# Kernel optimization log

Hardware: AMD Instinct MI355X
Metric: run time of the kernel (lower is better)

Reference implementation:

```python
import jax, jax.numpy as jnp
import numpy as np

EPS = 1e-10


def _sqdist(emb):
    # emb: [B, F, N]; pairwise squared distance over (eta, phi) rows 1:3
    coord = emb[:, 1:3, :]  # [B, 2, N]
    diff = coord[:, :, :, None] - coord[:, :, None, :]  # [B, 2, N, N]
    return jnp.sum(diff * diff, axis=1)  # [B, N, N]


def setup_inputs() -> dict:
    key = jax.random.key(0)
    k1, k2, k3 = jax.random.split(key, 3)
    B, F, N = 8, 6, 2048
    emb = jax.random.uniform(k1, (B, F, N), dtype=jnp.float32) + 0.1  # positive momenta
    alpha = 1.0 * (jax.random.uniform(k2, (1, 1), dtype=jnp.float32) * 0.02 + 0.99)
    beta = 1.0 * (jax.random.uniform(k3, (1, 1, 1), dtype=jnp.float32) * 0.02 + 0.99)
    return {"emb": emb, "alpha": alpha, "beta": beta}


def reference(emb, alpha, beta):
    # emb: [B, F, N]; alpha: [1,1]; beta: [1,1,1]
    sqdist = _sqdist(emb)                                  # [B, N, N]
    momentum = emb[:, 4, :] + EPS                          # [B, N]
    pow_momenta = jnp.exp(2.0 * alpha * jnp.log(momentum)) # p^(2*alpha), [B, N]
    # symmetric pairwise min: min(p_i^{2a}, p_j^{2a})
    min_momenta = jnp.minimum(pow_momenta[:, :, None], pow_momenta[:, None, :])  # [B, N, N]
    d_ij_alpha = sqdist * min_momenta
    d_ij_norm = -(beta ** 2) * d_ij_alpha                  # broadcast [1,1,1]
    # original unbind/cat/softmax/chunk/stack == row-wise softmax over last dim
    w_ij = jax.nn.softmax(d_ij_norm, axis=-1)
    return w_ij
```

## Files before the change

### kernel.cpp

```cpp
#include <hip/hip_runtime.h>

#define Nn   2048
#define BLK  256
#define TI   16
#define EPSf 1e-10f

typedef float f32x4 __attribute__((ext_vector_type(4)));

__global__ __launch_bounds__(BLK) void qcd_softmax_kernel(
    const float* __restrict__ emb,
    const float* __restrict__ alpha_p,
    const float* __restrict__ beta_p,
    float* __restrict__ out)
{
    __shared__ float s_cx[TI], s_cy[TI], s_q[TI];
    __shared__ float s_red[2][4];

    const int t  = threadIdx.x;
    const int b  = blockIdx.x >> 7;
    const int i0 = (blockIdx.x & 127) * TI;

    const float twoalpha = 2.0f * alpha_p[0];
    const float beta     = beta_p[0];
    const float nb2l2e   = -(beta * beta) * 1.4426950408889634f;

    const float* eb = emb + (size_t)b * 6 * Nn;

    const int j0 = t * 4;
    const int j1 = j0 + 1024;

    f32x4 cjx0 = *(const f32x4*)(eb + 1 * Nn + j0);
    f32x4 cjx1 = *(const f32x4*)(eb + 1 * Nn + j1);
    f32x4 cjy0 = *(const f32x4*)(eb + 2 * Nn + j0);
    f32x4 cjy1 = *(const f32x4*)(eb + 2 * Nn + j1);
    f32x4 mm0  = *(const f32x4*)(eb + 4 * Nn + j0);
    f32x4 mm1  = *(const f32x4*)(eb + 4 * Nn + j1);

    float qj0[4], qj1[4];
#pragma unroll
    for (int k = 0; k < 4; ++k) {
        qj0[k] = nb2l2e * expf(twoalpha * logf(mm0[k] + EPSf));
        qj1[k] = nb2l2e * expf(twoalpha * logf(mm1[k] + EPSf));
    }

    if (t < TI) {
        const int i = i0 + t;
        s_cx[t] = eb[1 * Nn + i];
        s_cy[t] = eb[2 * Nn + i];
        s_q[t]  = nb2l2e * expf(twoalpha * logf(eb[4 * Nn + i] + EPSf));
    }
    __syncthreads();

    const int wid  = t >> 6;
    const int lane = t & 63;

    for (int r = 0; r < TI; ++r) {
        const float cix = s_cx[r];
        const float ciy = s_cy[r];
        const float qi  = s_q[r];

        float e[8];
        float lsum = 0.f;
#pragma unroll
        for (int k = 0; k < 4; ++k) {
            const float dx = cjx0[k] - cix;
            const float dy = cjy0[k] - ciy;
            const float d2 = fmaf(dy, dy, dx * dx);
            e[k] = __builtin_amdgcn_exp2f(d2 * fmaxf(qj0[k], qi));
            lsum += e[k];
        }
#pragma unroll
        for (int k = 0; k < 4; ++k) {
            const float dx = cjx1[k] - cix;
            const float dy = cjy1[k] - ciy;
            const float d2 = fmaf(dy, dy, dx * dx);
            e[4 + k] = __builtin_amdgcn_exp2f(d2 * fmaxf(qj1[k], qi));
            lsum += e[4 + k];
        }

#pragma unroll
        for (int off = 32; off > 0; off >>= 1)
            lsum += __shfl_xor(lsum, off, 64);

        const int buf = r & 1;
        if (lane == 0) s_red[buf][wid] = lsum;
        __syncthreads();
        const float tot  = s_red[buf][0] + s_red[buf][1] + s_red[buf][2] + s_red[buf][3];
        const float rinv = 1.0f / tot;

        float* orow = out + (((size_t)b * Nn) + (size_t)(i0 + r)) * Nn;
        f32x4 o0, o1;
#pragma unroll
        for (int k = 0; k < 4; ++k) {
            o0[k] = e[k] * rinv;
            o1[k] = e[4 + k] * rinv;
        }
        __builtin_nontemporal_store(o0, (f32x4*)(orow + j0));
        __builtin_nontemporal_store(o1, (f32x4*)(orow + j1));
    }
}

extern "C" void kernel_launch(void* const* d_in, const int* in_sizes, int n_in,
                              void* d_out, int out_size, void* d_ws, size_t ws_size,
                              hipStream_t stream) {
    const float* emb   = (const float*)d_in[0];
    const float* alpha = (const float*)d_in[1];
    const float* beta  = (const float*)d_in[2];
    float* out         = (float*)d_out;

    dim3 grid(8 * (Nn / TI));
    dim3 block(BLK);
    qcd_softmax_kernel<<<grid, block, 0, stream>>>(emb, alpha, beta, out);
}
```

Baseline: 149.0 us.

## Assign whole rows per wavefront to drop block-level softmax reduction barriers

Each wavefront now owns four full output rows and holds all 2048 column coordinates and powered momenta in registers, so the row sum is reduced with wave shuffles only. This removes the shared-memory exchange and the __syncthreads per row. Nontemporal stores become plain stores, and launch bounds ask for two blocks per SIMD. The cost is much higher register use (96 floats of column state per thread) and the column exp/log setup repeated by every wave.

```diff
diff --git a/kernel.cpp b/kernel.cpp
--- a/kernel.cpp
+++ b/kernel.cpp
@@ -1,102 +1,87 @@
 #include <hip/hip_runtime.h>
 
 #define Nn   2048
-#define BLK  256
-#define TI   16
+#define NB   8
 #define EPSf 1e-10f
+#define RPW  4
+#define WPB  4
+#define BLK  (WPB * 64)
 
 typedef float f32x4 __attribute__((ext_vector_type(4)));
 
-__global__ __launch_bounds__(BLK) void qcd_softmax_kernel(
+__global__ __launch_bounds__(BLK, 2) void qcd_softmax_kernel(
     const float* __restrict__ emb,
     const float* __restrict__ alpha_p,
     const float* __restrict__ beta_p,
     float* __restrict__ out)
 {
-    __shared__ float s_cx[TI], s_cy[TI], s_q[TI];
-    __shared__ float s_red[2][4];
+    const int t    = threadIdx.x;
+    const int lane = t & 63;
+    const int w    = t >> 6;
+    const int b    = blockIdx.x >> 7;
+    const int i0   = (blockIdx.x & 127) * (RPW * WPB) + w * RPW;
 
-    const int t  = threadIdx.x;
-    const int b  = blockIdx.x >> 7;
-    const int i0 = (blockIdx.x & 127) * TI;
+    const float* eb  = emb + (size_t)b * 6 * Nn;
+    const float* cxp = eb + 1 * Nn;
+    const float* cyp = eb + 2 * Nn;
+    const float* mp  = eb + 4 * Nn;
 
     const float twoalpha = 2.0f * alpha_p[0];
     const float beta     = beta_p[0];
     const float nb2l2e   = -(beta * beta) * 1.4426950408889634f;
 
-    const float* eb = emb + (size_t)b * 6 * Nn;
-
-    const int j0 = t * 4;
-    const int j1 = j0 + 1024;
-
-    f32x4 cjx0 = *(const f32x4*)(eb + 1 * Nn + j0);
-    f32x4 cjx1 = *(const f32x4*)(eb + 1 * Nn + j1);
-    f32x4 cjy0 = *(const f32x4*)(eb + 2 * Nn + j0);
-    f32x4 cjy1 = *(const f32x4*)(eb + 2 * Nn + j1);
-    f32x4 mm0  = *(const f32x4*)(eb + 4 * Nn + j0);
-    f32x4 mm1  = *(const f32x4*)(eb + 4 * Nn + j1);
-
-    float qj0[4], qj1[4];
+    f32x4 cjx[8], cjy[8], qj[8];
 #pragma unroll
-    for (int k = 0; k < 4; ++k) {
-        qj0[k] = nb2l2e * expf(twoalpha * logf(mm0[k] + EPSf));
-        qj1[k] = nb2l2e * expf(twoalpha * logf(mm1[k] + EPSf));
+    for (int c = 0; c < 8; ++c) {
+        const int j = c * 256 + lane * 4;
+        cjx[c] = *(const f32x4*)(cxp + j);
+        cjy[c] = *(const f32x4*)(cyp + j);
+        const f32x4 m = *(const f32x4*)(mp + j);
+#pragma unroll
+        for (int k = 0; k < 4; ++k)
+            qj[c][k] = nb2l2e * expf(twoalpha * logf(m[k] + EPSf));
     }
 
-    if (t < TI) {
-        const int i = i0 + t;
-        s_cx[t] = eb[1 * Nn + i];
-        s_cy[t] = eb[2 * Nn + i];
-        s_q[t]  = nb2l2e * expf(twoalpha * logf(eb[4 * Nn + i] + EPSf));
-    }
-    __syncthreads();
+    const f32x4 cix4 = *(const f32x4*)(cxp + i0);
+    const f32x4 ciy4 = *(const f32x4*)(cyp + i0);
+    const f32x4 mi4  = *(const f32x4*)(mp + i0);
+    f32x4 qi4;
+#pragma unroll
+    for (int k = 0; k < 4; ++k)
+        qi4[k] = nb2l2e * expf(twoalpha * logf(mi4[k] + EPSf));
 
-    const int wid  = t >> 6;
-    const int lane = t & 63;
+#pragma unroll
+    for (int r = 0; r < RPW; ++r) {
+        const float cix = cix4[r];
+        const float ciy = ciy4[r];
+        const float qi  = qi4[r];
 
-    for (int r = 0; r < TI; ++r) {
-        const float cix = s_cx[r];
-        const float ciy = s_cy[r];
-        const float qi  = s_q[r];
-
-        float e[8];
+        f32x4 e[8];
         float lsum = 0.f;
 #pragma unroll
-        for (int k = 0; k < 4; ++k) {
-            const float dx = cjx0[k] - cix;
-            const float dy = cjy0[k] - ciy;
-            const float d2 = fmaf(dy, dy, dx * dx);
-            e[k] = __builtin_amdgcn_exp2f(d2 * fmaxf(qj0[k], qi));
-            lsum += e[k];
-        }
+        for (int c = 0; c < 8; ++c) {
+            const f32x4 dx = cjx[c] - cix;
+            const f32x4 dy = cjy[c] - ciy;
 #pragma unroll
-        for (int k = 0; k < 4; ++k) {
-            const float dx = cjx1[k] - cix;
-            const float dy = cjy1[k] - ciy;
-            const float d2 = fmaf(dy, dy, dx * dx);
-            e[4 + k] = __builtin_amdgcn_exp2f(d2 * fmaxf(qj1[k], qi));
-            lsum += e[4 + k];
+            for (int k = 0; k < 4; ++k) {
+                const float d2 = fmaf(dy[k], dy[k], dx[k] * dx[k]);
+                const float v  = __builtin_amdgcn_exp2f(d2 * fmaxf(qj[c][k], qi));
+                e[c][k] = v;
+                lsum += v;
+            }
         }
 
 #pragma unroll
         for (int off = 32; off > 0; off >>= 1)
             lsum += __shfl_xor(lsum, off, 64);
+        const float rinv = 1.0f / lsum;
 
-        const int buf = r & 1;
-        if (lane == 0) s_red[buf][wid] = lsum;
-        __syncthreads();
-        const float tot  = s_red[buf][0] + s_red[buf][1] + s_red[buf][2] + s_red[buf][3];
-        const float rinv = 1.0f / tot;
-
-        float* orow = out + (((size_t)b * Nn) + (size_t)(i0 + r)) * Nn;
-        f32x4 o0, o1;
+        float* orow = out + ((size_t)b * Nn + (i0 + r)) * Nn;
 #pragma unroll
-        for (int k = 0; k < 4; ++k) {
-            o0[k] = e[k] * rinv;
-            o1[k] = e[4 + k] * rinv;
+        for (int c = 0; c < 8; ++c) {
+            const f32x4 o = e[c] * rinv;
+            *(f32x4*)(orow + c * 256 + lane * 4) = o;
         }
-        __builtin_nontemporal_store(o0, (f32x4*)(orow + j0));
-        __builtin_nontemporal_store(o1, (f32x4*)(orow + j1));
     }
 }
 
@@ -108,7 +93,7 @@
     const float* beta  = (const float*)d_in[2];
     float* out         = (float*)d_out;
 
-    dim3 grid(8 * (Nn / TI));
     dim3 block(BLK);
+    dim3 grid(NB * (Nn / (RPW * WPB)));
     qcd_softmax_kernel<<<grid, block, 0, stream>>>(emb, alpha, beta, out);
 }
```

After: 144.1 us. 3.3% less time.
